# Kernel optimization log

Measured on AMD Instinct MI355X. Metric: run time of the kernel, lower is better.

## Reference

```python
import jax, jax.numpy as jnp
import numpy as np

B, N, ROWS, COLS = 32, 2048, 2, 2


def setup_inputs() -> dict:
    key = jax.random.key(0)
    kx, km, kc = jax.random.split(key, 3)
    x = jax.random.normal(kx, (B, N, N), dtype=jnp.float32)
    # kaiming_normal_ (fan_in mode, gain=sqrt(2)): std = sqrt(2/fan_in)
    Ms = jax.random.normal(km, (ROWS, COLS, N, N), dtype=jnp.float32) * np.sqrt(2.0 / N)
    coef = jax.random.normal(kc, (COLS, ROWS), dtype=jnp.float32) * np.sqrt(2.0 / ROWS)
    return {"x": x, "Ms": Ms, "coef": coef}


def reference(x, Ms, coef):
    rows, cols = Ms.shape[0], Ms.shape[1]
    # elementwise powers i**(c+1): (cols, B, N, N)
    xp = jnp.stack([x ** (c + 1) for c in range(cols)], axis=0)
    # trace(M @ X) == sum(M * X^T): O(N^2) per (b, r, c) instead of O(N^3)
    tr = jnp.einsum("rcij,cbji->brc", Ms, xp)  # (B, rows, cols)
    r_exp = jnp.arange(rows, dtype=tr.dtype)[None, :, None]
    ret = tr ** r_exp  # trace ** r  (r=0 -> 1.0, matching torch)
    ret = coef * ret  # (cols, rows) broadcasts against (B, rows, cols); rows==cols
    return jax.nn.sigmoid(ret.sum(axis=(1, 2)))
```

## Files before the change

kernel.cpp:

```cpp
#include <hip/hip_runtime.h>
#include <math.h>

#define NN    2048
#define BATCH 32
#define TILE  64
#define TPB   256
#define TPS   (NN / TILE)
#define NPOS  (TPS * TPS)
#define BGRP  8
#define BPG   (BATCH / BGRP)
#define GRID_MAIN (NPOS * BGRP)

#define WS_NEED ((size_t)BATCH * NPOS * sizeof(float))

template <int USE_WS>
__global__ __launch_bounds__(TPB) void trace_kernel(
    const float* __restrict__ x,
    const float* __restrict__ Ms,
    const float* __restrict__ coef,
    float* __restrict__ ws,
    float* __restrict__ out)
{
    __shared__ float xs[TILE][TILE + 1];
    __shared__ float wsum[TPB / 64];

    const int t    = threadIdx.x;
    const int pos  = blockIdx.x >> 3;
    const int grp  = blockIdx.x & (BGRP - 1);
    const int i0   = (pos / TPS) * TILE;
    const int j0   = (pos % TPS) * TILE;

    const int lane    = t & 63;
    const int wave    = t >> 6;
    const int jl      = t & 63;
    const int il_base = t >> 6;

    const float c2 = coef[2];
    const float c3 = coef[3];

    const float* __restrict__ M10 = Ms + (size_t)2 * NN * NN;
    const float* __restrict__ M11 = Ms + (size_t)3 * NN * NN;
    float m10[16], m11[16];
#pragma unroll
    for (int k = 0; k < 16; ++k) {
        const size_t off = (size_t)(i0 + il_base + 4 * k) * NN + (size_t)(j0 + jl);
        m10[k] = M10[off];
        m11[k] = M11[off];
    }

    const int sj  = t >> 4;
    const int si4 = (t & 15) * 4;

    for (int bb = 0; bb < BPG; ++bb) {
        const int b = grp * BPG + bb;
        const float* __restrict__ xb = x + (size_t)b * NN * NN;

#pragma unroll
        for (int k = 0; k < 4; ++k) {
            const int row = sj + 16 * k;
            const float4 v = *reinterpret_cast<const float4*>(
                xb + (size_t)(j0 + row) * NN + (size_t)(i0 + si4));
            xs[row][si4 + 0] = v.x;
            xs[row][si4 + 1] = v.y;
            xs[row][si4 + 2] = v.z;
            xs[row][si4 + 3] = v.w;
        }
        __syncthreads();

        float z = 0.f;
        {
            float s1 = 0.f, s2 = 0.f;
#pragma unroll
            for (int k = 0; k < 16; ++k) {
                const float v = xs[jl][il_base + 4 * k];
                s1 = fmaf(m10[k], v, s1);
                s2 = fmaf(m11[k], v * v, s2);
            }
            z = fmaf(c2, s1, c3 * s2);
        }

#pragma unroll
        for (int o = 32; o > 0; o >>= 1) z += __shfl_xor(z, o, 64);
        if (lane == 0) wsum[wave] = z;
        __syncthreads();

        if (t == 0) {
            const float zt = wsum[0] + wsum[1] + wsum[2] + wsum[3];
            if (USE_WS) {
                ws[(size_t)b * NPOS + pos] = zt;
            } else {
                atomicAdd(&out[b], zt);
            }
        }
    }
}

__global__ __launch_bounds__(TPB) void finalize_ws_kernel(
    const float* __restrict__ ws,
    const float* __restrict__ coef,
    float* __restrict__ out)
{
    __shared__ float wsum[TPB / 64];
    const int b = blockIdx.x;
    const int t = threadIdx.x;

    float s = 0.f;
#pragma unroll
    for (int m = 0; m < NPOS / TPB; ++m) s += ws[(size_t)b * NPOS + t + m * TPB];
#pragma unroll
    for (int o = 32; o > 0; o >>= 1) s += __shfl_xor(s, o, 64);
    if ((t & 63) == 0) wsum[t >> 6] = s;
    __syncthreads();
    if (t == 0) {
        const float z = coef[0] + coef[1] + wsum[0] + wsum[1] + wsum[2] + wsum[3];
        out[b] = 1.0f / (1.0f + expf(-z));
    }
}

__global__ void init_out_kernel(float* __restrict__ out)
{
    if (threadIdx.x < BATCH) out[threadIdx.x] = 0.f;
}

__global__ void finalize_atomic_kernel(const float* __restrict__ coef,
                                       float* __restrict__ out)
{
    const int b = threadIdx.x;
    if (b < BATCH) {
        const float z = coef[0] + coef[1] + out[b];
        out[b] = 1.0f / (1.0f + expf(-z));
    }
}

extern "C" void kernel_launch(void* const* d_in, const int* in_sizes, int n_in,
                              void* d_out, int out_size, void* d_ws, size_t ws_size,
                              hipStream_t stream) {
    const float* x    = (const float*)d_in[0];
    const float* Ms   = (const float*)d_in[1];
    const float* coef = (const float*)d_in[2];
    float* out = (float*)d_out;
    float* ws  = (float*)d_ws;

    if (ws_size >= WS_NEED) {
        trace_kernel<1><<<GRID_MAIN, TPB, 0, stream>>>(x, Ms, coef, ws, out);
        finalize_ws_kernel<<<BATCH, TPB, 0, stream>>>(ws, coef, out);
    } else {
        init_out_kernel<<<1, 64, 0, stream>>>(out);
        trace_kernel<0><<<GRID_MAIN, TPB, 0, stream>>>(x, Ms, coef, ws, out);
        finalize_atomic_kernel<<<1, 64, 0, stream>>>(coef, out);
    }
}
```

Before: 749.8 us.

## Drop LDS transpose and batch all x loads per block into registers

Each thread now keeps a transposed patch of M (4 j-rows by 4 i-columns) in registers, so the float4 reads of x line up directly with the matching M elements and the shared-memory transpose with its per-batch barriers goes away. All four batch slices are loaded up front as independent float4 loads, and the four wave reductions run together with a single barrier at the end. This exposes more memory-level parallelism in a bandwidth-bound kernel. In exchange, the M reads become strided scalar loads (column reads across i rows), which may coalesce worse, and register pressure goes up.

```diff
diff --git a/kernel.cpp b/kernel.cpp
--- a/kernel.cpp
+++ b/kernel.cpp
@@ -21,8 +21,7 @@
     float* __restrict__ ws,
     float* __restrict__ out)
 {
-    __shared__ float xs[TILE][TILE + 1];
-    __shared__ float wsum[TPB / 64];
+    __shared__ float wsum[TPB / 64][BPG];
 
     const int t    = threadIdx.x;
     const int pos  = blockIdx.x >> 3;
@@ -30,67 +29,77 @@
     const int i0   = (pos / TPS) * TILE;
     const int j0   = (pos % TPS) * TILE;
 
-    const int lane    = t & 63;
-    const int wave    = t >> 6;
-    const int jl      = t & 63;
-    const int il_base = t >> 6;
+    const int lane = t & 63;
+    const int wave = t >> 6;
+    const int il4  = (t & 15) * 4;
+    const int jrb  = t >> 4;
 
     const float c2 = coef[2];
     const float c3 = coef[3];
 
     const float* __restrict__ M10 = Ms + (size_t)2 * NN * NN;
     const float* __restrict__ M11 = Ms + (size_t)3 * NN * NN;
-    float m10[16], m11[16];
+    float m10t[4][4], m11t[4][4];
 #pragma unroll
-    for (int k = 0; k < 16; ++k) {
-        const size_t off = (size_t)(i0 + il_base + 4 * k) * NN + (size_t)(j0 + jl);
-        m10[k] = M10[off];
-        m11[k] = M11[off];
+    for (int p = 0; p < 4; ++p) {
+        const int j = j0 + jrb + 16 * p;
+#pragma unroll
+        for (int c = 0; c < 4; ++c) {
+            const size_t off = (size_t)(i0 + il4 + c) * NN + (size_t)j;
+            m10t[p][c] = M10[off];
+            m11t[p][c] = M11[off];
+        }
     }
 
-    const int sj  = t >> 4;
-    const int si4 = (t & 15) * 4;
+    const float* __restrict__ xbase =
+        x + ((size_t)grp * BPG) * NN * NN + (size_t)j0 * NN + (size_t)(i0 + il4);
 
-    for (int bb = 0; bb < BPG; ++bb) {
-        const int b = grp * BPG + bb;
-        const float* __restrict__ xb = x + (size_t)b * NN * NN;
+    float s1[BPG], s2[BPG];
+#pragma unroll
+    for (int bb = 0; bb < BPG; ++bb) { s1[bb] = 0.f; s2[bb] = 0.f; }
 
 #pragma unroll
-        for (int k = 0; k < 4; ++k) {
-            const int row = sj + 16 * k;
-            const float4 v = *reinterpret_cast<const float4*>(
-                xb + (size_t)(j0 + row) * NN + (size_t)(i0 + si4));
-            xs[row][si4 + 0] = v.x;
-            xs[row][si4 + 1] = v.y;
-            xs[row][si4 + 2] = v.z;
-            xs[row][si4 + 3] = v.w;
+    for (int p = 0; p < 4; ++p) {
+        const size_t rowoff = (size_t)(jrb + 16 * p) * NN;
+        float4 v[BPG];
+#pragma unroll
+        for (int bb = 0; bb < BPG; ++bb)
+            v[bb] = *reinterpret_cast<const float4*>(
+                xbase + (size_t)bb * NN * NN + rowoff);
+#pragma unroll
+        for (int bb = 0; bb < BPG; ++bb) {
+            s1[bb] = fmaf(m10t[p][0], v[bb].x, s1[bb]);
+            s1[bb] = fmaf(m10t[p][1], v[bb].y, s1[bb]);
+            s1[bb] = fmaf(m10t[p][2], v[bb].z, s1[bb]);
+            s1[bb] = fmaf(m10t[p][3], v[bb].w, s1[bb]);
+            s2[bb] = fmaf(m11t[p][0], v[bb].x * v[bb].x, s2[bb]);
+            s2[bb] = fmaf(m11t[p][1], v[bb].y * v[bb].y, s2[bb]);
+            s2[bb] = fmaf(m11t[p][2], v[bb].z * v[bb].z, s2[bb]);
+            s2[bb] = fmaf(m11t[p][3], v[bb].w * v[bb].w, s2[bb]);
         }
-        __syncthreads();
+    }
 
-        float z = 0.f;
-        {
-            float s1 = 0.f, s2 = 0.f;
+    float z[BPG];
 #pragma unroll
-            for (int k = 0; k < 16; ++k) {
-                const float v = xs[jl][il_base + 4 * k];
-                s1 = fmaf(m10[k], v, s1);
-                s2 = fmaf(m11[k], v * v, s2);
-            }
-            z = fmaf(c2, s1, c3 * s2);
-        }
+    for (int bb = 0; bb < BPG; ++bb) z[bb] = fmaf(c2, s1[bb], c3 * s2[bb]);
+#pragma unroll
+    for (int o = 32; o > 0; o >>= 1) {
+#pragma unroll
+        for (int bb = 0; bb < BPG; ++bb) z[bb] += __shfl_xor(z[bb], o, 64);
+    }
+    if (lane == 0) {
+#pragma unroll
+        for (int bb = 0; bb < BPG; ++bb) wsum[wave][bb] = z[bb];
+    }
+    __syncthreads();
 
-#pragma unroll
-        for (int o = 32; o > 0; o >>= 1) z += __shfl_xor(z, o, 64);
-        if (lane == 0) wsum[wave] = z;
-        __syncthreads();
-
-        if (t == 0) {
-            const float zt = wsum[0] + wsum[1] + wsum[2] + wsum[3];
-            if (USE_WS) {
-                ws[(size_t)b * NPOS + pos] = zt;
-            } else {
-                atomicAdd(&out[b], zt);
-            }
+    if (t < BPG) {
+        const float zt = wsum[0][t] + wsum[1][t] + wsum[2][t] + wsum[3][t];
+        const int b = grp * BPG + t;
+        if (USE_WS) {
+            ws[(size_t)b * NPOS + pos] = zt;
+        } else {
+            atomicAdd(&out[b], zt);
         }
     }
 }
```

Result: slower. 784.5 us (+4.6%).
